# Optimization experiments

Measured on AMD Instinct MI355X. Metric: run time of the kernel, lower is better.

## Reference

```python
import jax, jax.numpy as jnp
import numpy as np

# Module hyperparameters (from init_kwargs)
L = 32        # spatial length
CIN = 128     # in_channels
COUT = 256    # out_channels
N = 8         # num_filters
STRIDE = 1
K = 9         # kernel_size (l//4+1 default for l>16)


def setup_inputs() -> dict:
    key = jax.random.key(0)
    kx, kw = jax.random.split(key)
    x = jax.random.normal(kx, (32, CIN, L, L), dtype=jnp.float32)
    # weight init: uniform in [-r, r], r = sqrt(1/(cin*k*k)), shape (n, cin//8, k, k)
    r = np.sqrt(1.0 / (CIN * K * K)).astype(np.float32)
    weight = (jax.random.uniform(kw, (N, CIN // 8, K, K), dtype=jnp.float32) - 0.5) * 2.0 * r
    return {"x": x, "weight": weight}


def reference(x, weight):
    # 3D real FFT over (channel, H, W) of the input: [B, CIN, L, L//2+1] complex
    x_hat = jnp.fft.rfftn(x, axes=(1, 2, 3))
    # Zero-pad weight (cin//8 -> CIN, k -> L) and transform: [N, CIN, L, L//2+1]
    w_hat = jnp.fft.rfftn(weight, s=(CIN, L, L))
    # Broadcast multiply (no channel reduction): [B, N, CIN, L, L//2+1]
    freq_out = jnp.einsum('bchw,nchw->bnchw', x_hat, w_hat)
    # Inverse 3D real FFT over (channel, H, W): [B, N, CIN, L, L]
    out = jnp.fft.irfftn(freq_out, axes=(2, 3, 4))
    # Channel shrink: keep every shrink_ratio-th channel -> CIN/shrink = COUT/N channels
    shrink_ratio = N * CIN // COUT
    out = out[:, :, ::shrink_ratio]                       # [B, N, COUT//N, L, L]
    out = out.reshape(out.shape[0], -1, out.shape[3], out.shape[4])  # [B, COUT, L, L]
    if STRIDE == 2:
        out = out[:, :, ::2, ::2]
    return out
```

## Files before the change

kernel.cpp:

```cpp
#include <hip/hip_runtime.h>

typedef __attribute__((ext_vector_type(4)))  float f32x4;
typedef __attribute__((ext_vector_type(16))) float f32x16;
typedef __attribute__((ext_vector_type(8)))  short s16x8;

#define KK 9
#define NCHUNK 23

__device__ inline unsigned short f2bf(float f) {
    union { float f; unsigned int u; } v; v.f = f;
    unsigned int u = v.u + 0x7FFFu + ((v.u >> 16) & 1u);
    return (unsigned short)(u >> 16);
}


__global__ void prep_w32(const float* __restrict__ wgt, unsigned short* __restrict__ Bg) {
    int idx = blockIdx.x * 256 + threadIdx.x;
    if (idx >= 108 * 64 * 8) return;
    int e     = idx & 7;
    int lanei = (idx >> 3) & 63;
    int chunk = idx >> 9;
    int col   = lanei & 31;
    int khalf = lanei >> 5;
    int n  = col & 7;
    int p  = col >> 3;
    int kx = chunk / 12;
    int s  = chunk - 12 * kx;
    int ky = s - 3 + p;
    int cp = khalf * 8 + e;
    int dc = 15 - cp;
    float val = 0.f;
    if (ky >= 0 && ky <= 8)
        val = wgt[((n * 16 + dc) * KK + ky) * KK + kx];
    Bg[idx] = f2bf(val);
}

__global__ __launch_bounds__(512, 4) void fconv_mfma32(
    const float* __restrict__ x,
    const unsigned short* __restrict__ Bg,
    float* __restrict__ out)
{
    __shared__ char smb[65536];

    const int tid = threadIdx.x;
    const int wg  = ((blockIdx.x & 7) << 6) + (blockIdx.x >> 3);
    const int b   = wg >> 4;
    const int jp  = wg & 15;

    const float* xb = x + ((size_t)b << 17);
    #pragma unroll
    for (int t = 0; t < 2; ++t) {
        const int j = jp + t * 16;
        int choff[16];
        #pragma unroll
        for (int i = 0; i < 16; ++i)
            choff[i] = ((4 * j - 15 + i) & 127) << 10;

        #pragma unroll
        for (int i = 0; i < 2; ++i) {
            int cell = i * 512 + tid;
            #pragma unroll
            for (int h = 0; h < 2; ++h) {
                union { unsigned short u16[8]; uint4 v; } pk;
                #pragma unroll
                for (int e = 0; e < 8; ++e)
                    pk.u16[e] = f2bf(xb[choff[h * 8 + e] + cell]);
                *(uint4*)(smb + t * 32768 + h * 16384 + cell * 16) = pk.v;
            }
        }
    }
    __syncthreads();

    const int lane  = tid & 63;
    const int wave  = tid >> 6;
    const int pr    = wave & 3;
    const int t     = wave >> 2;
    const int wrow  = lane & 31;
    const int khalf = lane >> 5;
    const int g8    = pr * 8;

    f32x16 acc0 = (f32x16)0.f;
    f32x16 acc1 = (f32x16)0.f;
    const char* bp    = (const char*)Bg + (lane << 4);
    const char* abuf  = smb + t * 32768 + (khalf << 14);

    #pragma unroll 1
    for (int kx = 0; kx < 9; ++kx) {
        const char* ab  = abuf + (((wrow - kx) & 31) << 4);
        const char* bpk = bp + kx * 12288;

        s16x8 bb[12];
        #pragma unroll
        for (int s = 0; s < 12; ++s)
            bb[s] = *(const s16x8*)(bpk + (s << 10));

        #pragma unroll
        for (int rr = 0; rr < 16; ++rr) {
            int R = (g8 - 8 + rr) & 31;
            s16x8 a = *(const s16x8*)(ab + (R << 9));
            if (rr <= 11)
                acc0 = __builtin_amdgcn_mfma_f32_32x32x16_bf16(a, bb[11 - rr], acc0, 0, 0, 0);
            if (rr >= 4)
                acc1 = __builtin_amdgcn_mfma_f32_32x32x16_bf16(a, bb[15 - rr], acc1, 0, 0, 0);
        }
    }

    const int n  = wrow & 7;
    const int p  = wrow >> 3;
    const int jj = jp + t * 16;
    {
        float* ob = out + (((size_t)(b * 256 + n * 32 + jj)) << 10)
                        + ((g8 + p) << 5) + 4 * khalf;
        #pragma unroll
        for (int q = 0; q < 4; ++q) {
            f32x4 v = { acc0[4*q], acc0[4*q+1], acc0[4*q+2], acc0[4*q+3] };
            *(f32x4*)(ob + q * 8) = v;
        }
    }
    {
        float* ob = out + (((size_t)(b * 256 + n * 32 + jj)) << 10)
                        + ((g8 + 4 + p) << 5) + 4 * khalf;
        #pragma unroll
        for (int q = 0; q < 4; ++q) {
            f32x4 v = { acc1[4*q], acc1[4*q+1], acc1[4*q+2], acc1[4*q+3] };
            *(f32x4*)(ob + q * 8) = v;
        }
    }
}

__global__ void prep_w(const float* __restrict__ wgt, unsigned short* __restrict__ Bg) {
    int idx = blockIdx.x * 256 + threadIdx.x;
    if (idx >= NCHUNK * 4 * 16 * 8) return;
    int e   = idx & 7;
    int col = (idx >> 3) & 15;
    int g   = (idx >> 7) & 3;
    int c   = idx >> 9;
    int pi   = g >> 1;
    int half = g & 1;
    int cp = half * 8 + e;
    int dc = 15 - cp;
    int q  = 2 * c + pi;
    int n  = col & 7;
    int t  = col >> 3;
    float val = 0.f;
    if (q <= 44) {
        int ky2 = q / 9;
        int kx  = q - 9 * ky2;
        int ky  = 2 * ky2 + t;
        if (ky <= 8)
            val = wgt[((n * 16 + dc) * KK + ky) * KK + kx];
    }
    Bg[idx] = f2bf(val);
}

__global__ __launch_bounds__(256) void fconv_mfma(
    const float* __restrict__ x,
    const unsigned short* __restrict__ Bg,
    float* __restrict__ out)
{
    __shared__ char smem[32768 + 4096];
    char*  smb     = smem;
    float* handoff = (float*)(smem + 32768);

    const int tid = threadIdx.x;
    const int b   = blockIdx.x >> 5;
    const int j   = blockIdx.x & 31;

    const float* xb = x + ((size_t)b << 17);
    int choff[16];
    #pragma unroll
    for (int i = 0; i < 16; ++i)
        choff[i] = ((4 * j - 15 + i) & 127) << 10;

    #pragma unroll
    for (int i = 0; i < 4; ++i) {
        int cell = i * 256 + tid;
        #pragma unroll
        for (int h = 0; h < 2; ++h) {
            union { unsigned short u16[8]; uint4 v; } pk;
            #pragma unroll
            for (int e = 0; e < 8; ++e)
                pk.u16[e] = f2bf(xb[choff[h * 8 + e] + cell]);
            *(uint4*)(smb + h * 16384 + cell * 16) = pk.v;
        }
    }
    __syncthreads();

    const int lane = tid & 63;
    const int wave = tid >> 6;
    const int r    = lane & 15;
    const int g    = lane >> 4;
    const int half = g & 1;
    const int pi   = g >> 1;
    const int y0   = wave * 8;

    f32x4 acc[8][2];
    #pragma unroll
    for (int dy = 0; dy < 8; ++dy) { acc[dy][0] = (f32x4)0.f; acc[dy][1] = (f32x4)0.f; }

    const char* bptr = (const char*)Bg + ((g * 16 + r) << 4);
    s16x8 bfrag = *(const s16x8*)(bptr);

    #pragma unroll 1
    for (int c = 0; c < NCHUNK; ++c) {
        int q   = 2 * c + pi;
        int ky2 = q / 9;
        int kx  = q - 9 * ky2;
        int wr  = (r - kx) & 31;
        int yb  = (y0 - 2 * ky2) & 31;
        int abase = (half << 14) + (wr << 4);

        int cn = (c < NCHUNK - 1) ? c + 1 : NCHUNK - 1;
        s16x8 bnext = *(const s16x8*)(bptr + (cn << 10));

        #pragma unroll
        for (int dy = 0; dy < 8; ++dy) {
            int yy = (yb + dy) & 31;
            int ra = abase + (yy << 9);
            s16x8 a0 = *(const s16x8*)(smb + ra);
            s16x8 a1 = *(const s16x8*)(smb + (ra ^ 256));
            acc[dy][0] = __builtin_amdgcn_mfma_f32_16x16x32_bf16(a0, bfrag, acc[dy][0], 0, 0, 0);
            acc[dy][1] = __builtin_amdgcn_mfma_f32_16x16x32_bf16(a1, bfrag, acc[dy][1], 0, 0, 0);
        }
        bfrag = bnext;
    }

    float recv[8][2][4];
    #pragma unroll
    for (int dy = 0; dy < 8; ++dy)
        #pragma unroll
        for (int h = 0; h < 2; ++h)
            #pragma unroll
            for (int i = 0; i < 4; ++i)
                recv[dy][h][i] = __shfl_xor(acc[dy][h][i], 8);

    if (r < 8) {
        #pragma unroll
        for (int h = 0; h < 2; ++h)
            *(f32x4*)&handoff[wave * 256 + r * 32 + h * 16 + g * 4] = *(f32x4*)recv[7][h];
    }
    __syncthreads();

    if (r < 8) {
        const int pw = (wave + 3) & 3;
        f32x4 prev[2];
        #pragma unroll
        for (int h = 0; h < 2; ++h)
            prev[h] = *(f32x4*)&handoff[pw * 256 + r * 32 + h * 16 + g * 4];

        float* ob = out + (((size_t)(b * 256 + r * 32 + j)) << 10) + (g << 2);
        #pragma unroll
        for (int dy = 0; dy < 8; ++dy) {
            #pragma unroll
            for (int h = 0; h < 2; ++h) {
                f32x4 t1 = (dy == 0) ? prev[h] : *(f32x4*)recv[dy - 1][h];
                f32x4 v  = acc[dy][h] + t1;
                *(f32x4*)(ob + (y0 + dy) * 32 + h * 16) = v;
            }
        }
    }
}

__global__ __launch_bounds__(256, 2) void fconv_fallback(
    const float* __restrict__ x,
    const float* __restrict__ wgt,
    float* __restrict__ out)
{
    __shared__ float sw[16 * KK * KK * 8];
    const int tid = threadIdx.x;
    for (int idx = tid; idx < 8 * 16 * KK * KK; idx += 256) {
        int n  = idx / (16 * KK * KK);
        int rm = idx - n * (16 * KK * KK);
        int dc = rm / (KK * KK);
        int r2 = rm - dc * (KK * KK);
        int ky = r2 / KK;
        int kx = r2 - ky * KK;
        sw[((dc * KK + kx) * KK + ky) * 8 + n] = wgt[idx];
    }
    __syncthreads();

    const int bid = blockIdx.x;
    const int b   = bid >> 6;
    const int j   = (bid >> 1) & 31;
    const int yh  = bid & 1;
    const int xw  = tid & 31;
    const int yg  = tid >> 5;
    const int y_base = yh * 16 + yg * 2;

    int rows[10];
    #pragma unroll
    for (int i = 0; i < 10; ++i)
        rows[i] = ((y_base + 24 + i) & 31) << 5;

    float acc[8][2];
    #pragma unroll
    for (int n = 0; n < 8; ++n) { acc[n][0] = 0.f; acc[n][1] = 0.f; }

    const int c0 = 4 * j;
    #pragma unroll 1
    for (int dc = 0; dc < 16; ++dc) {
        const int c_src = (c0 - dc) & 127;
        const float* bx = x + (((size_t)b * 128 + c_src) << 10);
        #pragma unroll 1
        for (int kx = 0; kx < KK; ++kx) {
            const int x_col = (xw - kx) & 31;
            float win[10];
            #pragma unroll
            for (int i = 0; i < 10; ++i)
                win[i] = bx[rows[i] + x_col];
            const float4* wp = (const float4*)&sw[((dc * KK + kx) * KK) * 8];
            #pragma unroll
            for (int ky = 0; ky < KK; ++ky) {
                float4 wA = wp[2 * ky];
                float4 wB = wp[2 * ky + 1];
                float x0 = win[8 - ky];
                float x1 = win[9 - ky];
                acc[0][0] += x0 * wA.x; acc[0][1] += x1 * wA.x;
                acc[1][0] += x0 * wA.y; acc[1][1] += x1 * wA.y;
                acc[2][0] += x0 * wA.z; acc[2][1] += x1 * wA.z;
                acc[3][0] += x0 * wA.w; acc[3][1] += x1 * wA.w;
                acc[4][0] += x0 * wB.x; acc[4][1] += x1 * wB.x;
                acc[5][0] += x0 * wB.y; acc[5][1] += x1 * wB.y;
                acc[6][0] += x0 * wB.z; acc[6][1] += x1 * wB.z;
                acc[7][0] += x0 * wB.w; acc[7][1] += x1 * wB.w;
            }
        }
    }
    #pragma unroll
    for (int n = 0; n < 8; ++n) {
        float* op = out + ((((size_t)b * 256) + n * 32 + j) << 10) + (y_base << 5) + xw;
        op[0]  = acc[n][0];
        op[32] = acc[n][1];
    }
}

extern "C" void kernel_launch(void* const* d_in, const int* in_sizes, int n_in,
                              void* d_out, int out_size, void* d_ws, size_t ws_size,
                              hipStream_t stream) {
    const float* x   = (const float*)d_in[0];
    const float* w   = (const float*)d_in[1];
    float*       out = (float*)d_out;

    const size_t BG32_BYTES = (size_t)108 * 64 * 8 * sizeof(unsigned short);
    const size_t BG16_BYTES = (size_t)NCHUNK * 4 * 16 * 8 * sizeof(unsigned short);

    if (ws_size >= BG32_BYTES) {
        unsigned short* Bg = (unsigned short*)d_ws;
        prep_w32<<<216, 256, 0, stream>>>(w, Bg);
        fconv_mfma32<<<512, 512, 0, stream>>>(x, Bg, out);
    } else if (ws_size >= BG16_BYTES) {
        unsigned short* Bg = (unsigned short*)d_ws;
        prep_w<<<46, 256, 0, stream>>>(w, Bg);
        fconv_mfma<<<1024, 256, 0, stream>>>(x, Bg, out);
    } else {
        fconv_fallback<<<2048, 256, 0, stream>>>(x, w, out);
    }
}
```

Before: 110.1 us.

## Vectorize input staging loads and software-pipeline B loads with MFMA in main loop

Input staging now loads float2 pairs, converts them with packed bf16 conversion, and splits them into two shared-memory rows with byte permutes, halving the global load instruction count. The main kx loop is manually scheduled: half the B fragments are prefetched for the next iteration while MFMAs run, A loads are interleaved with MFMAs, and s_setprio raises wave priority around MFMA bursts. The aim is to hide global and LDS latency behind matrix work, at the cost of more registers and a hand-fixed instruction order.

```diff
diff --git a/kernel.cpp b/kernel.cpp
--- a/kernel.cpp
+++ b/kernel.cpp
@@ -1,4 +1,5 @@
 #include <hip/hip_runtime.h>
+#include <hip/hip_bf16.h>
 
 typedef __attribute__((ext_vector_type(4)))  float f32x4;
 typedef __attribute__((ext_vector_type(16))) float f32x16;
@@ -48,25 +49,37 @@
     const int jp  = wg & 15;
 
     const float* xb = x + ((size_t)b << 17);
-    #pragma unroll
-    for (int t = 0; t < 2; ++t) {
-        const int j = jp + t * 16;
+    const int cell = tid * 2;
+    #pragma unroll
+    for (int tt = 0; tt < 2; ++tt) {
+        const int j = jp + tt * 16;
         int choff[16];
         #pragma unroll
         for (int i = 0; i < 16; ++i)
             choff[i] = ((4 * j - 15 + i) & 127) << 10;
 
         #pragma unroll
-        for (int i = 0; i < 2; ++i) {
-            int cell = i * 512 + tid;
-            #pragma unroll
-            for (int h = 0; h < 2; ++h) {
-                union { unsigned short u16[8]; uint4 v; } pk;
-                #pragma unroll
-                for (int e = 0; e < 8; ++e)
-                    pk.u16[e] = f2bf(xb[choff[h * 8 + e] + cell]);
-                *(uint4*)(smb + t * 32768 + h * 16384 + cell * 16) = pk.v;
+        for (int h = 0; h < 2; ++h) {
+            unsigned int u[8];
+            #pragma unroll
+            for (int e = 0; e < 8; ++e) {
+                float2 v = *(const float2*)(xb + choff[h * 8 + e] + cell);
+                union { __hip_bfloat162 h2; unsigned int u32; } cv;
+                cv.h2 = __float22bfloat162_rn(v);
+                u[e] = cv.u32;
             }
+            uint4 lo, hi;
+            lo.x = __builtin_amdgcn_perm(u[1], u[0], 0x05040100u);
+            lo.y = __builtin_amdgcn_perm(u[3], u[2], 0x05040100u);
+            lo.z = __builtin_amdgcn_perm(u[5], u[4], 0x05040100u);
+            lo.w = __builtin_amdgcn_perm(u[7], u[6], 0x05040100u);
+            hi.x = __builtin_amdgcn_perm(u[1], u[0], 0x07060302u);
+            hi.y = __builtin_amdgcn_perm(u[3], u[2], 0x07060302u);
+            hi.z = __builtin_amdgcn_perm(u[5], u[4], 0x07060302u);
+            hi.w = __builtin_amdgcn_perm(u[7], u[6], 0x07060302u);
+            char* wp = smb + tt * 32768 + h * 16384 + cell * 16;
+            *(uint4*)(wp)      = lo;
+            *(uint4*)(wp + 16) = hi;
         }
     }
     __syncthreads();
@@ -81,29 +94,59 @@
 
     f32x16 acc0 = (f32x16)0.f;
     f32x16 acc1 = (f32x16)0.f;
-    const char* bp    = (const char*)Bg + (lane << 4);
-    const char* abuf  = smb + t * 32768 + (khalf << 14);
+    const char* bp   = (const char*)Bg + (lane << 4);
+    const char* abuf = smb + t * 32768 + (khalf << 14);
+
+    #define BLD(dst, kxv, s)  dst = *(const s16x8*)(bp + ((((kxv) * 12 + (s)) << 10)))
+    #define ALD(dst, rr)      dst = *(const s16x8*)(ab + (((g8 - 8 + (rr)) & 31) << 9))
+    #define M0(a_, b_) acc0 = __builtin_amdgcn_mfma_f32_32x32x16_bf16(a_, b_, acc0, 0, 0, 0)
+    #define M1(a_, b_) acc1 = __builtin_amdgcn_mfma_f32_32x32x16_bf16(a_, b_, acc1, 0, 0, 0)
+
+    s16x8 bbl0, bbl1, bbl2, bbl3, bbl4, bbl5;
+    s16x8 bbh0, bbh1, bbh2, bbh3, bbh4, bbh5;
+    BLD(bbl0, 0, 6);  BLD(bbl1, 0, 7);  BLD(bbl2, 0, 8);
+    BLD(bbl3, 0, 9);  BLD(bbl4, 0, 10); BLD(bbl5, 0, 11);
 
     #pragma unroll 1
     for (int kx = 0; kx < 9; ++kx) {
-        const char* ab  = abuf + (((wrow - kx) & 31) << 4);
-        const char* bpk = bp + kx * 12288;
-
-        s16x8 bb[12];
-        #pragma unroll
-        for (int s = 0; s < 12; ++s)
-            bb[s] = *(const s16x8*)(bpk + (s << 10));
-
-        #pragma unroll
-        for (int rr = 0; rr < 16; ++rr) {
-            int R = (g8 - 8 + rr) & 31;
-            s16x8 a = *(const s16x8*)(ab + (R << 9));
-            if (rr <= 11)
-                acc0 = __builtin_amdgcn_mfma_f32_32x32x16_bf16(a, bb[11 - rr], acc0, 0, 0, 0);
-            if (rr >= 4)
-                acc1 = __builtin_amdgcn_mfma_f32_32x32x16_bf16(a, bb[15 - rr], acc1, 0, 0, 0);
-        }
-    }
+        const char* ab = abuf + (((wrow - kx) & 31) << 4);
+        const int  kxn = (kx < 8) ? kx + 1 : 8;
+
+        BLD(bbh0, kx, 0); BLD(bbh1, kx, 1); BLD(bbh2, kx, 2);
+        BLD(bbh3, kx, 3); BLD(bbh4, kx, 4); BLD(bbh5, kx, 5);
+
+        s16x8 a0, a1, a2, a3, a4, a5, ak0, ak1, ak2, ak3;
+        ALD(a0, 0); ALD(a1, 1); ALD(a2, 2); ALD(a3, 3);
+        __builtin_amdgcn_s_setprio(1);
+        M0(a0, bbl5); M0(a1, bbl4);
+        ALD(a4, 4); ALD(a5, 5);
+        M0(a2, bbl3); M0(a3, bbl2);
+        ALD(ak0, 6); ALD(ak1, 7);
+        M0(a4, bbl1); M1(a4, bbl5);
+        ALD(ak2, 8); ALD(ak3, 9);
+        M0(a5, bbl0); M1(a5, bbl4);
+        M1(ak0, bbl3); M1(ak1, bbl2); M1(ak2, bbl1); M1(ak3, bbl0);
+        __builtin_amdgcn_s_setprio(0);
+
+        BLD(bbl0, kxn, 6);  BLD(bbl1, kxn, 7);  BLD(bbl2, kxn, 8);
+        BLD(bbl3, kxn, 9);  BLD(bbl4, kxn, 10); BLD(bbl5, kxn, 11);
+
+        s16x8 b0, b1, b2, b3, b4, b5;
+        ALD(b0, 10); ALD(b1, 11);
+        __builtin_amdgcn_s_setprio(1);
+        M0(ak0, bbh5); M0(ak1, bbh4);
+        ALD(b2, 12); ALD(b3, 13);
+        M0(ak2, bbh3); M0(ak3, bbh2);
+        ALD(b4, 14); ALD(b5, 15);
+        M0(b0, bbh1); M0(b1, bbh0);
+        M1(b0, bbh5); M1(b1, bbh4); M1(b2, bbh3);
+        M1(b3, bbh2); M1(b4, bbh1); M1(b5, bbh0);
+        __builtin_amdgcn_s_setprio(0);
+    }
+    #undef BLD
+    #undef ALD
+    #undef M0
+    #undef M1
 
     const int n  = wrow & 7;
     const int p  = wrow >> 3;
```

New measurement: 100.2 us. 9.0% less time.
